# Kernel tuning notes

Hardware: AMD Instinct MI355X
Metric: run time of the kernel (lower is better)

## Reference

```python
import jax, jax.numpy as jnp
import numpy as np

N_NODES = 50000


def gcn_layer(x, src, dst, ew, W, b, n_nodes):
    # PyG GCNConv: add self-loops (weight 1), symmetric deg^-1/2 normalization,
    # linear transform, scatter-add aggregation at destination, then bias.
    loop = jnp.arange(n_nodes, dtype=src.dtype)
    s = jnp.concatenate([src, loop])
    d = jnp.concatenate([dst, loop])
    w = jnp.concatenate([ew, jnp.ones((n_nodes,), dtype=ew.dtype)])
    deg = jax.ops.segment_sum(w, d, num_segments=n_nodes)  # [N]
    dinv = jnp.where(deg > 0, jax.lax.rsqrt(jnp.where(deg > 0, deg, 1.0)), 0.0)
    norm = dinv[s] * w * dinv[d]  # [E+N]
    h = x @ W  # [N, out]
    msg = h[s] * norm[:, None]  # gather + scale, [E+N, out]
    out = jax.ops.segment_sum(msg, d, num_segments=n_nodes)  # scatter-add
    return out + b


def setup_inputs() -> dict:
    key = jax.random.key(0)
    k1, k2, k3, k4, k5, k6, k7 = jax.random.split(key, 7)
    N, E, C_IN, C_OUT = N_NODES, 600000, 128, 128
    x = jax.random.normal(k1, (N, C_IN), dtype=jnp.float32)
    edge_index = jax.random.randint(k2, (2, E), 0, N, dtype=jnp.int64)
    edge_weight = jax.random.uniform(k3, (E,), dtype=jnp.float32)
    # Glorot-style init like PyG's Linear default
    s1 = 1.0 / np.sqrt(C_IN)
    s2 = 1.0 / np.sqrt(C_OUT)
    W1 = jax.random.uniform(k4, (C_IN, C_OUT), jnp.float32, -s1, s1)
    b1 = jnp.zeros((C_OUT,), dtype=jnp.float32)
    W2 = jax.random.uniform(k5, (C_OUT, C_OUT), jnp.float32, -s2, s2)
    b2 = jnp.zeros((C_OUT,), dtype=jnp.float32)
    return {"x": x, "edge_index": edge_index, "edge_weight": edge_weight,
            "W1": W1, "b1": b1, "W2": W2, "b2": b2}


def reference(x, edge_index, edge_weight, W1, b1, W2, b2):
    src, dst = edge_index[0], edge_index[1]
    h = jax.nn.relu(gcn_layer(x, src, dst, edge_weight, W1, b1, N_NODES))
    return jax.nn.relu(gcn_layer(h, src, dst, edge_weight, W2, b2, N_NODES))
```

## Files before the change

kernel.cpp:

```cpp
#include <hip/hip_runtime.h>
#include <math.h>

#define CH   128
#define CH4  32
#define TPB  256
#define SCANB 1024
#define WIMG 16384
#define NREP 8

typedef __attribute__((ext_vector_type(8))) short short8;
typedef __attribute__((ext_vector_type(4))) float floatx4;
typedef __attribute__((ext_vector_type(8))) float float8;

static __device__ __forceinline__ unsigned short f2bf(float f) {
    unsigned u = __float_as_uint(f);
    return (unsigned short)((u + 0x7fffu + ((u >> 16) & 1u)) >> 16);
}
static __device__ __forceinline__ float bf2f(unsigned short s) {
    return __uint_as_float(((unsigned)s) << 16);
}
static __device__ __forceinline__ float8 bf8_to_f8(short8 u) {
    float8 f;
    #pragma unroll
    for (int i = 0; i < 8; ++i) f[i] = bf2f((unsigned short)u[i]);
    return f;
}

__global__ void k_prep(const float* __restrict__ W1, const float* __restrict__ W2,
                       short* __restrict__ Wsplit, float4* __restrict__ zbase,
                       int nzero4, int nbPrep) {
    int bx = blockIdx.x;
    if (bx >= nbPrep) {
        int i = (bx - nbPrep) * TPB + threadIdx.x;
        if (i < nzero4) zbase[i] = make_float4(0.f, 0.f, 0.f, 0.f);
        return;
    }
    int i = bx * TPB + threadIdx.x;
    if (i >= 2 * CH * CH) return;
    int layer = i >> 14;
    int idx   = i & 16383;
    int k = idx >> 7, c = idx & 127;
    float w = (layer ? W2 : W1)[k * CH + c];
    unsigned short hi = f2bf(w);
    unsigned short lo = f2bf(w - bf2f(hi));
    int colh = c >> 6, nn = c & 63;
    int kt = k >> 5, q = (k & 31) >> 3, j = k & 7;
    int ns = nn >> 4, ln = q * 16 + (nn & 15);
    size_t base = (size_t)(layer * 2 + colh) * WIMG;
    size_t off  = ((size_t)(kt * 4 + ns) * 64 + ln) * 8 + j;
    Wsplit[base + off]        = (short)hi;
    Wsplit[base + 8192 + off] = (short)lo;
}

static __device__ __forceinline__ void gemm_body_f32(
        const float* __restrict__ X, const short* __restrict__ Wfrag,
        unsigned short* __restrict__ H, int n, int tile, int colh, int tid) {
    __shared__ __align__(16) short sW[2][4][4][64][8];
    {
        const float4* gsrc = (const float4*)Wfrag;
        float4* ldst = (float4*)sW;
        #pragma unroll
        for (int i = 0; i < 8; ++i)
            ldst[i * TPB + tid] = gsrc[i * TPB + tid];
    }
    __syncthreads();

    const int lane = tid & 63;
    const int wv   = tid >> 6;
    const int q    = lane >> 4;
    const int m    = lane & 15;
    const int row0 = tile * 64 + wv * 16;
    if (row0 >= n) return;

    int rrow = row0 + m;
    if (rrow > n - 1) rrow = n - 1;

    const float4* xr = (const float4*)(X + (size_t)rrow * CH);
    float4 xa[4][2];
    #pragma unroll
    for (int kt = 0; kt < 4; ++kt) {
        xa[kt][0] = xr[kt * 8 + q * 2 + 0];
        xa[kt][1] = xr[kt * 8 + q * 2 + 1];
    }

    floatx4 acc[4];
    #pragma unroll
    for (int ns = 0; ns < 4; ++ns) acc[ns] = (floatx4){0.f, 0.f, 0.f, 0.f};

    #pragma unroll
    for (int kt = 0; kt < 4; ++kt) {
        float xf[8] = { xa[kt][0].x, xa[kt][0].y, xa[kt][0].z, xa[kt][0].w,
                        xa[kt][1].x, xa[kt][1].y, xa[kt][1].z, xa[kt][1].w };
        short8 ah, al;
        #pragma unroll
        for (int j = 0; j < 8; ++j) {
            float v = xf[j];
            unsigned short h = f2bf(v);
            ah[j] = (short)h;
            al[j] = (short)f2bf(v - bf2f(h));
        }
        #pragma unroll
        for (int ns = 0; ns < 4; ++ns) {
            short8 bh = *(const short8*)&sW[0][kt][ns][lane][0];
            short8 bl = *(const short8*)&sW[1][kt][ns][lane][0];
            acc[ns] = __builtin_amdgcn_mfma_f32_16x16x32_bf16(ah, bh, acc[ns], 0, 0, 0);
            acc[ns] = __builtin_amdgcn_mfma_f32_16x16x32_bf16(al, bh, acc[ns], 0, 0, 0);
            acc[ns] = __builtin_amdgcn_mfma_f32_16x16x32_bf16(ah, bl, acc[ns], 0, 0, 0);
        }
    }

    #pragma unroll
    for (int ns = 0; ns < 4; ++ns) {
        #pragma unroll
        for (int reg = 0; reg < 4; ++reg) {
            int r = row0 + q * 4 + reg;
            if (r < n)
                H[(size_t)r * CH + colh * 64 + ns * 16 + m] = f2bf(acc[ns][reg]);
        }
    }
}

__global__ __launch_bounds__(TPB, 4)
void k_gemm_rank(const float* __restrict__ X, const short* __restrict__ Wsplit,
                 unsigned short* __restrict__ H, int n,
                 const int* __restrict__ dst, int* __restrict__ counts_rep,
                 int* __restrict__ rank, int E, int nbE4, int Np) {
    int bx = blockIdx.x;
    if (bx < nbE4) {
        int stride = nbE4 * TPB;
        int e = bx * TPB + threadIdx.x;
        #pragma unroll
        for (int it = 0; it < 4; ++it, e += stride) {
            if (e < E) {
                int d = dst[e];
                if ((unsigned)d < (unsigned)n) {
                    int rep = e & (NREP - 1);
                    rank[e] = atomicAdd(&counts_rep[rep * Np + d], 1);
                }
            }
        }
    } else {
        bx -= nbE4;
        int colh = bx & 1;
        gemm_body_f32(X, Wsplit + (size_t)colh * WIMG, H, n, bx >> 1, colh,
                      threadIdx.x);
    }
}

__global__ __launch_bounds__(TPB, 4)
void k_gemm_bf(const unsigned short* __restrict__ X, const short* __restrict__ Wsplit,
               const float* __restrict__ dinv, unsigned short* __restrict__ H, int n) {
    __shared__ __align__(16) short sW[4][4][64][8];
    const int tid  = threadIdx.x;
    const int colh = (int)blockIdx.x & 1;
    const int tile = (int)blockIdx.x >> 1;
    {
        const float4* gsrc = (const float4*)(Wsplit + (size_t)colh * WIMG);
        float4* ldst = (float4*)sW;
        #pragma unroll
        for (int i = 0; i < 4; ++i)
            ldst[i * TPB + tid] = gsrc[i * TPB + tid];
    }
    __syncthreads();

    const int lane = tid & 63;
    const int wv   = tid >> 6;
    const int q    = lane >> 4;
    const int m    = lane & 15;
    const int row0 = tile * 64 + wv * 16;
    if (row0 >= n) return;

    int rrow = row0 + m;
    if (rrow > n - 1) rrow = n - 1;

    const short8* xr8 = (const short8*)(X + (size_t)rrow * CH);
    short8 a[4];
    #pragma unroll
    for (int kt = 0; kt < 4; ++kt) a[kt] = xr8[kt * 4 + q];

    floatx4 acc[4];
    #pragma unroll
    for (int ns = 0; ns < 4; ++ns) acc[ns] = (floatx4){0.f, 0.f, 0.f, 0.f};

    #pragma unroll
    for (int kt = 0; kt < 4; ++kt) {
        #pragma unroll
        for (int ns = 0; ns < 4; ++ns) {
            short8 bh = *(const short8*)&sW[kt][ns][lane][0];
            acc[ns] = __builtin_amdgcn_mfma_f32_16x16x32_bf16(a[kt], bh, acc[ns], 0, 0, 0);
        }
    }

    float dr[4];
    #pragma unroll
    for (int reg = 0; reg < 4; ++reg) {
        int r = row0 + q * 4 + reg;
        dr[reg] = (r < n) ? dinv[r] : 0.f;
    }
    #pragma unroll
    for (int ns = 0; ns < 4; ++ns) {
        #pragma unroll
        for (int reg = 0; reg < 4; ++reg) {
            int r = row0 + q * 4 + reg;
            if (r < n)
                H[(size_t)r * CH + colh * 64 + ns * 16 + m] =
                    f2bf(acc[ns][reg] * dr[reg]);
        }
    }
}

__global__ __launch_bounds__(SCANB)
void k_scan1(const int* __restrict__ counts_rep, int Np,
             int* __restrict__ counts_tot, int* __restrict__ repoff8,
             int* __restrict__ row_start, int* __restrict__ partials,
             int* __restrict__ pp_s, int* __restrict__ done, int nb, int n) {
    __shared__ int s[SCANB];
    __shared__ int slast;
    int gid = blockIdx.x * SCANB + threadIdx.x;
    int c[NREP];
    int v = 0;
    #pragma unroll
    for (int r = 0; r < NREP; ++r) {
        c[r] = (gid < n) ? counts_rep[r * Np + gid] : 0;
        v += c[r];
    }
    s[threadIdx.x] = v;
    __syncthreads();
    for (int off = 1; off < SCANB; off <<= 1) {
        int t = (threadIdx.x >= off) ? s[threadIdx.x - off] : 0;
        __syncthreads();
        s[threadIdx.x] += t;
        __syncthreads();
    }
    if (gid < n) {
        row_start[gid]  = s[threadIdx.x] - v;
        counts_tot[gid] = v;
        int pre = 0;
        int ro[NREP];
        #pragma unroll
        for (int r = 0; r < NREP; ++r) { ro[r] = pre; pre += c[r]; }
        ((int4*)repoff8)[gid * 2 + 0] = make_int4(ro[0], ro[1], ro[2], ro[3]);
        ((int4*)repoff8)[gid * 2 + 1] = make_int4(ro[4], ro[5], ro[6], ro[7]);
    }
    if (threadIdx.x == SCANB - 1) {
        partials[blockIdx.x] = s[SCANB - 1];
        __threadfence();
        int old = atomicAdd(done, 1);
        slast = (old == nb - 1);
    }
    __syncthreads();
    if (slast && threadIdx.x < 64) {
        int pv = (threadIdx.x < nb) ? atomicAdd(&partials[threadIdx.x], 0) : 0;
        int inc = pv;
        #pragma unroll
        for (int off = 1; off < 64; off <<= 1) {
            int t = __shfl_up(inc, off, 64);
            if ((threadIdx.x & 63) >= off) inc += t;
        }
        if (threadIdx.x < nb) pp_s[threadIdx.x] = inc - pv;
    }
}

__global__ void k_fill(const int* __restrict__ src, const int* __restrict__ dst,
                       const float* __restrict__ ew, const int* __restrict__ row_start,
                       const int* __restrict__ pp_s, const int* __restrict__ repoff8,
                       const int* __restrict__ rank, int2* __restrict__ edges,
                       int E, int n) {
    int e = blockIdx.x * blockDim.x + threadIdx.x;
    if (e >= E) return;
    int s = src[e], d = dst[e];
    if ((unsigned)s >= (unsigned)n || (unsigned)d >= (unsigned)n) return;
    int rep = e & (NREP - 1);
    int base = row_start[d] + pp_s[d >> 10] + repoff8[d * NREP + rep];
    edges[base + rank[e]] = make_int2(s, __float_as_int(ew[e]));
}

__global__ __launch_bounds__(TPB)
void k_deg_scale(const int* __restrict__ row_start, const int* __restrict__ pp_s,
                 const int* __restrict__ counts, const int2* __restrict__ edges,
                 float* __restrict__ dinv, unsigned short* __restrict__ h, int n) {
    int t = blockIdx.x * blockDim.x + threadIdx.x;
    int node = t >> 4;
    if (node >= n) return;
    int tx = t & 15;
    int j0  = row_start[node] + pp_s[node >> 10];
    int cnt = counts[node];
    float sum = 0.f;
    for (int j = tx; j < cnt; j += 16)
        sum += __int_as_float(edges[j0 + j].y);
    #pragma unroll
    for (int off = 8; off; off >>= 1) sum += __shfl_down(sum, off, 16);
    float di = rsqrtf(1.0f + __shfl(sum, 0, 16));
    if (tx == 0) dinv[node] = di;
    short8* hp = (short8*)h + (size_t)node * 16 + tx;
    short8 v = *hp;
    short8 o;
    #pragma unroll
    for (int c = 0; c < 8; ++c)
        o[c] = (short)f2bf(bf2f((unsigned short)v[c]) * di);
    *hp = o;
}

static __device__ __forceinline__ float8 agg_node8(
        const short8* __restrict__ h8, const int2* __restrict__ edges,
        float di, const float8 b, int node, int tx,
        const int* __restrict__ row_start, const int* __restrict__ pp_s,
        const int* __restrict__ counts) {
    float8 hv = bf8_to_f8(h8[(size_t)node * 16 + tx]);
    float8 acc;
    #pragma unroll
    for (int i = 0; i < 8; ++i) acc[i] = 0.f;

    int j   = row_start[node] + pp_s[node >> 10];
    int end = j + counts[node];

    for (; j + 8 <= end; j += 8) {
        int2 e[8];
        #pragma unroll
        for (int i = 0; i < 8; ++i) e[i] = edges[j + i];
        short8 g[8];
        #pragma unroll
        for (int i = 0; i < 8; ++i) g[i] = h8[(size_t)e[i].x * 16 + tx];
        #pragma unroll
        for (int i = 0; i < 8; ++i) {
            float w = __int_as_float(e[i].y);
            float8 gf = bf8_to_f8(g[i]);
            #pragma unroll
            for (int c = 0; c < 8; ++c) acc[c] += gf[c] * w;
        }
    }
    if (j + 4 <= end) {
        int2 e[4];
        #pragma unroll
        for (int i = 0; i < 4; ++i) e[i] = edges[j + i];
        short8 g[4];
        #pragma unroll
        for (int i = 0; i < 4; ++i) g[i] = h8[(size_t)e[i].x * 16 + tx];
        #pragma unroll
        for (int i = 0; i < 4; ++i) {
            float w = __int_as_float(e[i].y);
            float8 gf = bf8_to_f8(g[i]);
            #pragma unroll
            for (int c = 0; c < 8; ++c) acc[c] += gf[c] * w;
        }
        j += 4;
    }
    for (; j < end; ++j) {
        int2 e0 = edges[j];
        float w0 = __int_as_float(e0.y);
        float8 gf = bf8_to_f8(h8[(size_t)e0.x * 16 + tx]);
        #pragma unroll
        for (int c = 0; c < 8; ++c) acc[c] += gf[c] * w0;
    }

    float8 o;
    #pragma unroll
    for (int c = 0; c < 8; ++c) o[c] = di * (hv[c] + acc[c]) + b[c];
    return o;
}

__global__ __launch_bounds__(TPB)
void k_aggregate1(const unsigned short* __restrict__ h,
                  const int* __restrict__ row_start, const int* __restrict__ pp_s,
                  const int* __restrict__ counts, const int2* __restrict__ edges,
                  const float* __restrict__ dinv, const float* __restrict__ bias,
                  unsigned short* __restrict__ out, int n) {
    int t = blockIdx.x * blockDim.x + threadIdx.x;
    int node = t >> 4;
    if (node >= n) return;
    int tx = t & 15;
    float8 b;
    #pragma unroll
    for (int c = 0; c < 8; ++c) b[c] = bias[tx * 8 + c];
    float8 o = agg_node8((const short8*)h, edges, dinv[node], b, node, tx,
                         row_start, pp_s, counts);
    short8 u;
    #pragma unroll
    for (int c = 0; c < 8; ++c) u[c] = (short)f2bf(fmaxf(o[c], 0.f));
    ((short8*)out)[(size_t)node * 16 + tx] = u;
}

__global__ __launch_bounds__(TPB)
void k_aggregate2(const unsigned short* __restrict__ h,
                  const int* __restrict__ row_start, const int* __restrict__ pp_s,
                  const int* __restrict__ counts, const int2* __restrict__ edges,
                  const float* __restrict__ dinv, const float* __restrict__ bias,
                  float* __restrict__ out, int n) {
    int t = blockIdx.x * blockDim.x + threadIdx.x;
    int node = t >> 4;
    if (node >= n) return;
    int tx = t & 15;
    float8 b;
    #pragma unroll
    for (int c = 0; c < 8; ++c) b[c] = bias[tx * 8 + c];
    float8 o = agg_node8((const short8*)h, edges, dinv[node], b, node, tx,
                         row_start, pp_s, counts);
    float4 lo = make_float4(fmaxf(o[0], 0.f), fmaxf(o[1], 0.f),
                            fmaxf(o[2], 0.f), fmaxf(o[3], 0.f));
    float4 hi = make_float4(fmaxf(o[4], 0.f), fmaxf(o[5], 0.f),
                            fmaxf(o[6], 0.f), fmaxf(o[7], 0.f));
    ((float4*)out)[(size_t)node * CH4 + tx * 2 + 0] = lo;
    ((float4*)out)[(size_t)node * CH4 + tx * 2 + 1] = hi;
}

extern "C" void kernel_launch(void* const* d_in, const int* in_sizes, int n_in,
                              void* d_out, int out_size, void* d_ws, size_t ws_size,
                              hipStream_t stream) {
    const float* x  = (const float*)d_in[0];
    const int*   ei = (const int*)d_in[1];
    const float* ew = (const float*)d_in[2];
    const float* W1 = (const float*)d_in[3];
    const float* b1 = (const float*)d_in[4];
    const float* W2 = (const float*)d_in[5];
    const float* b2 = (const float*)d_in[6];
    float* out = (float*)d_out;

    const int N = in_sizes[0] / CH;
    const int E = in_sizes[2];
    const int* src = ei;
    const int* dst = ei + E;

    size_t Np = ((size_t)N + 255) & ~(size_t)255;
    size_t Ep = ((size_t)E + 63) & ~(size_t)63;
    float* ws          = (float*)d_ws;
    float* dinv        = ws;
    unsigned short* h  = (unsigned short*)(dinv + Np);
    unsigned short* o1 = h + (size_t)N * CH;
    unsigned short* h2 = o1 + (size_t)N * CH;
    int*   counts_rep  = (int*)(h2 + (size_t)N * CH);
    int*   done        = counts_rep + NREP * Np;
    int    nzero4      = (int)((NREP * Np + 64) / 4);
    int*  counts_tot   = done + 64;
    int*  row_start    = counts_tot + Np;
    int*  repoff8      = row_start + Np;
    int*  rank         = repoff8 + NREP * Np;
    int*  partials     = rank + Ep;
    int*  pp_s         = partials + 64;
    int2* edges        = (int2*)(pp_s + 64);
    short* Wsplit      = (short*)(edges + E);

    const int nbE    = (E + TPB - 1) / TPB;
    const int nbE4   = (E + TPB * 4 - 1) / (TPB * 4);
    const int nbAgg  = (int)(((size_t)N * 16 + TPB - 1) / TPB);
    const int nbScan = (N + SCANB - 1) / SCANB;
    const int nbGemm2 = 2 * ((N + 63) / 64);
    const int nbPrep  = (2 * CH * CH + TPB - 1) / TPB;
    const int nbZero  = (nzero4 + TPB - 1) / TPB;

    k_prep     <<<nbPrep + nbZero, TPB, 0, stream>>>(W1, W2, Wsplit,
                                                     (float4*)counts_rep,
                                                     nzero4, nbPrep);

    k_gemm_rank<<<nbE4 + nbGemm2, TPB, 0, stream>>>(x, Wsplit, h, N, dst,
                                                    counts_rep, rank, E, nbE4, (int)Np);
    k_scan1    <<<nbScan, SCANB, 0, stream>>>(counts_rep, (int)Np, counts_tot,
                                              repoff8, row_start, partials,
                                              pp_s, done, nbScan, N);
    k_fill     <<<nbE, TPB, 0, stream>>>(src, dst, ew, row_start, pp_s, repoff8,
                                         rank, edges, E, N);
    k_deg_scale<<<nbAgg, TPB, 0, stream>>>(row_start, pp_s, counts_tot, edges,
                                           dinv, h, N);

    k_aggregate1<<<nbAgg, TPB, 0, stream>>>(h, row_start, pp_s, counts_tot,
                                            edges, dinv, b1, o1, N);
    k_gemm_bf   <<<nbGemm2, TPB, 0, stream>>>(o1, Wsplit + 2 * (size_t)WIMG,
                                              dinv, h2, N);
    k_aggregate2<<<nbAgg, TPB, 0, stream>>>(h2, row_start, pp_s, counts_tot,
                                            edges, dinv, b2, out, N);
}
```

Baseline: 216.6 us.

## Compute degrees via atomics in rank pass and fold source dinv into edge weights

Edge-weight degree sums are accumulated with replicated float atomics alongside the counting pass, and dinv is computed in the scan kernel. The separate degree/scale kernel that rescaled h is removed. The source-side normalization is now baked into the stored edge weight in the fill pass, and the self-loop term uses di squared in aggregation. The GEMM2 epilogue drops the dinv scaling. This saves one kernel launch and a full read/write of h, at the cost of extra float atomics, a dinv gather per edge in fill, and non-deterministic float summation order.

```diff
diff --git a/kernel.cpp b/kernel.cpp
--- a/kernel.cpp
+++ b/kernel.cpp
@@ -123,7 +123,8 @@
 __global__ __launch_bounds__(TPB, 4)
 void k_gemm_rank(const float* __restrict__ X, const short* __restrict__ Wsplit,
                  unsigned short* __restrict__ H, int n,
-                 const int* __restrict__ dst, int* __restrict__ counts_rep,
+                 const int* __restrict__ dst, const float* __restrict__ ew,
+                 int* __restrict__ counts_rep, float* __restrict__ degsum_rep,
                  int* __restrict__ rank, int E, int nbE4, int Np) {
     int bx = blockIdx.x;
     if (bx < nbE4) {
@@ -136,6 +137,7 @@
                 if ((unsigned)d < (unsigned)n) {
                     int rep = e & (NREP - 1);
                     rank[e] = atomicAdd(&counts_rep[rep * Np + d], 1);
+                    atomicAdd(&degsum_rep[rep * Np + d], ew[e]);
                 }
             }
         }
@@ -149,7 +151,7 @@
 
 __global__ __launch_bounds__(TPB, 4)
 void k_gemm_bf(const unsigned short* __restrict__ X, const short* __restrict__ Wsplit,
-               const float* __restrict__ dinv, unsigned short* __restrict__ H, int n) {
+               unsigned short* __restrict__ H, int n) {
     __shared__ __align__(16) short sW[4][4][64][8];
     const int tid  = threadIdx.x;
     const int colh = (int)blockIdx.x & 1;
@@ -191,29 +193,23 @@
         }
     }
 
-    float dr[4];
-    #pragma unroll
-    for (int reg = 0; reg < 4; ++reg) {
-        int r = row0 + q * 4 + reg;
-        dr[reg] = (r < n) ? dinv[r] : 0.f;
-    }
     #pragma unroll
     for (int ns = 0; ns < 4; ++ns) {
         #pragma unroll
         for (int reg = 0; reg < 4; ++reg) {
             int r = row0 + q * 4 + reg;
             if (r < n)
-                H[(size_t)r * CH + colh * 64 + ns * 16 + m] =
-                    f2bf(acc[ns][reg] * dr[reg]);
+                H[(size_t)r * CH + colh * 64 + ns * 16 + m] = f2bf(acc[ns][reg]);
         }
     }
 }
 
 __global__ __launch_bounds__(SCANB)
-void k_scan1(const int* __restrict__ counts_rep, int Np,
-             int* __restrict__ counts_tot, int* __restrict__ repoff8,
-             int* __restrict__ row_start, int* __restrict__ partials,
-             int* __restrict__ pp_s, int* __restrict__ done, int nb, int n) {
+void k_scan1(const int* __restrict__ counts_rep, const float* __restrict__ degsum_rep,
+             int Np, int* __restrict__ counts_tot, int* __restrict__ repoff8,
+             int* __restrict__ row_start, float* __restrict__ dinv,
+             int* __restrict__ partials, int* __restrict__ pp_s,
+             int* __restrict__ done, int nb, int n) {
     __shared__ int s[SCANB];
     __shared__ int slast;
     int gid = blockIdx.x * SCANB + threadIdx.x;
@@ -235,6 +231,10 @@
     if (gid < n) {
         row_start[gid]  = s[threadIdx.x] - v;
         counts_tot[gid] = v;
+        float ds = 0.f;
+        #pragma unroll
+        for (int r = 0; r < NREP; ++r) ds += degsum_rep[r * Np + gid];
+        dinv[gid] = rsqrtf(1.0f + ds);
         int pre = 0;
         int ro[NREP];
         #pragma unroll
@@ -264,41 +264,15 @@
 __global__ void k_fill(const int* __restrict__ src, const int* __restrict__ dst,
                        const float* __restrict__ ew, const int* __restrict__ row_start,
                        const int* __restrict__ pp_s, const int* __restrict__ repoff8,
-                       const int* __restrict__ rank, int2* __restrict__ edges,
-                       int E, int n) {
+                       const int* __restrict__ rank, const float* __restrict__ dinv,
+                       int2* __restrict__ edges, int E, int n) {
     int e = blockIdx.x * blockDim.x + threadIdx.x;
     if (e >= E) return;
     int s = src[e], d = dst[e];
     if ((unsigned)s >= (unsigned)n || (unsigned)d >= (unsigned)n) return;
     int rep = e & (NREP - 1);
     int base = row_start[d] + pp_s[d >> 10] + repoff8[d * NREP + rep];
-    edges[base + rank[e]] = make_int2(s, __float_as_int(ew[e]));
-}
-
-__global__ __launch_bounds__(TPB)
-void k_deg_scale(const int* __restrict__ row_start, const int* __restrict__ pp_s,
-                 const int* __restrict__ counts, const int2* __restrict__ edges,
-                 float* __restrict__ dinv, unsigned short* __restrict__ h, int n) {
-    int t = blockIdx.x * blockDim.x + threadIdx.x;
-    int node = t >> 4;
-    if (node >= n) return;
-    int tx = t & 15;
-    int j0  = row_start[node] + pp_s[node >> 10];
-    int cnt = counts[node];
-    float sum = 0.f;
-    for (int j = tx; j < cnt; j += 16)
-        sum += __int_as_float(edges[j0 + j].y);
-    #pragma unroll
-    for (int off = 8; off; off >>= 1) sum += __shfl_down(sum, off, 16);
-    float di = rsqrtf(1.0f + __shfl(sum, 0, 16));
-    if (tx == 0) dinv[node] = di;
-    short8* hp = (short8*)h + (size_t)node * 16 + tx;
-    short8 v = *hp;
-    short8 o;
-    #pragma unroll
-    for (int c = 0; c < 8; ++c)
-        o[c] = (short)f2bf(bf2f((unsigned short)v[c]) * di);
-    *hp = o;
+    edges[base + rank[e]] = make_int2(s, __float_as_int(ew[e] * dinv[s]));
 }
 
 static __device__ __forceinline__ float8 agg_node8(
@@ -353,9 +327,10 @@
         for (int c = 0; c < 8; ++c) acc[c] += gf[c] * w0;
     }
 
+    float di2 = di * di;
     float8 o;
     #pragma unroll
-    for (int c = 0; c < 8; ++c) o[c] = di * (hv[c] + acc[c]) + b[c];
+    for (int c = 0; c < 8; ++c) o[c] = di2 * hv[c] + di * acc[c] + b[c];
     return o;
 }
 
@@ -428,8 +403,9 @@
     unsigned short* o1 = h + (size_t)N * CH;
     unsigned short* h2 = o1 + (size_t)N * CH;
     int*   counts_rep  = (int*)(h2 + (size_t)N * CH);
-    int*   done        = counts_rep + NREP * Np;
-    int    nzero4      = (int)((NREP * Np + 64) / 4);
+    float* degsum_rep  = (float*)(counts_rep + NREP * Np);
+    int*   done        = (int*)(degsum_rep + NREP * Np);
+    int    nzero4      = (int)((2 * NREP * Np + 64) / 4);
     int*  counts_tot   = done + 64;
     int*  row_start    = counts_tot + Np;
     int*  repoff8      = row_start + Np;
@@ -451,20 +427,20 @@
                                                      (float4*)counts_rep,
                                                      nzero4, nbPrep);
 
-    k_gemm_rank<<<nbE4 + nbGemm2, TPB, 0, stream>>>(x, Wsplit, h, N, dst,
-                                                    counts_rep, rank, E, nbE4, (int)Np);
-    k_scan1    <<<nbScan, SCANB, 0, stream>>>(counts_rep, (int)Np, counts_tot,
-                                              repoff8, row_start, partials,
-                                              pp_s, done, nbScan, N);
+    k_gemm_rank<<<nbE4 + nbGemm2, TPB, 0, stream>>>(x, Wsplit, h, N, dst, ew,
+                                                    counts_rep, degsum_rep,
+                                                    rank, E, nbE4, (int)Np);
+    k_scan1    <<<nbScan, SCANB, 0, stream>>>(counts_rep, degsum_rep, (int)Np,
+                                              counts_tot, repoff8, row_start,
+                                              dinv, partials, pp_s, done,
+                                              nbScan, N);
     k_fill     <<<nbE, TPB, 0, stream>>>(src, dst, ew, row_start, pp_s, repoff8,
-                                         rank, edges, E, N);
-    k_deg_scale<<<nbAgg, TPB, 0, stream>>>(row_start, pp_s, counts_tot, edges,
-                                           dinv, h, N);
+                                         rank, dinv, edges, E, N);
 
     k_aggregate1<<<nbAgg, TPB, 0, stream>>>(h, row_start, pp_s, counts_tot,
                                             edges, dinv, b1, o1, N);
     k_gemm_bf   <<<nbGemm2, TPB, 0, stream>>>(o1, Wsplit + 2 * (size_t)WIMG,
-                                              dinv, h2, N);
+                                              h2, N);
     k_aggregate2<<<nbAgg, TPB, 0, stream>>>(h2, row_start, pp_s, counts_tot,
                                             edges, dinv, b2, out, N);
 }
```

New measurement: 235.5 us. 1.09x slower.
